# Performance work log

Hardware: AMD Instinct MI355X
Metric: run time of the kernel (lower is better)

## Reference

```python
import jax, jax.numpy as jnp
import numpy as np

WINDOW = 11
SIGMA = 1.5
C_IN = 3
PAD = WINDOW // 2
ALPHA_CHARB, ALPHA_MSE, ALPHA_SSIM = 0.3, 0.1, 0.6
EPS = 1e-6
C1 = (0.01 * 1) ** 2
C2 = (0.03 * 1) ** 2


def _gaussian_kernel():
    # 1D gaussian -> outer product -> depthwise weight [C, 1, K, K]
    x = np.arange(-(WINDOW // 2), WINDOW // 2 + 1, dtype=np.float32)
    w = np.exp(-0.5 * x * x / (SIGMA * SIGMA))
    w = w / w.sum()
    k2d = np.outer(w, w).astype(np.float32)  # [K, K]
    return jnp.asarray(np.tile(k2d[None, None], (C_IN, 1, 1, 1)))  # [C,1,K,K]

_KERNEL = _gaussian_kernel()


def _gauss_filter(x):
    # depthwise conv, NCHW / OIHW, SAME-style padding of K//2
    return jax.lax.conv_general_dilated(
        x, _KERNEL,
        window_strides=(1, 1),
        padding=[(PAD, PAD), (PAD, PAD)],
        dimension_numbers=('NCHW', 'OIHW', 'NCHW'),
        feature_group_count=C_IN,
    )


def setup_inputs() -> dict:
    key = jax.random.key(0)
    k1, k2 = jax.random.split(key)
    shape = (16, 3, 512, 512)
    pred = jax.random.uniform(k1, shape, dtype=jnp.float32)
    target = jax.random.uniform(k2, shape, dtype=jnp.float32)
    return {"pred": pred, "target": target}


def reference(pred, target):
    # SSIM map
    mu_x = _gauss_filter(pred)
    mu_y = _gauss_filter(target)
    sigma2_x = _gauss_filter(pred * pred) - mu_x * mu_x
    sigma2_y = _gauss_filter(target * target) - mu_y * mu_y
    sigma_xy = _gauss_filter(pred * target) - mu_x * mu_y
    A1 = 2.0 * mu_x * mu_y + C1
    A2 = 2.0 * sigma_xy + C2
    B1 = mu_x * mu_x + mu_y * mu_y + C1
    B2 = sigma2_x + sigma2_y + C2
    ssim = (A1 / B1) * (A2 / B2)

    diff = pred - target
    charb = jnp.sqrt(diff * diff + EPS * EPS)
    mse = diff * diff * 20.0
    ssim_loss = 1.0 - ssim
    return ALPHA_CHARB * charb + ALPHA_MSE * mse + ALPHA_SSIM * ssim_loss
```

## Files before the change

### kernel.cpp

```cpp
#include <hip/hip_runtime.h>


#define IMG    512
#define RAD    5
#define KW     11
#define STRH   32
#define NSTEP  (STRH + 2 * RAD)
#define ROWE   74
#define PLANE  (IMG * IMG)

#define C1F  1e-4f
#define C2F  9e-4f
#define EPS2 1e-12f

#define W0 0.00102838f
#define W1 0.00759876f
#define W2 0.03600076f
#define W3 0.10936067f
#define W4 0.21300537f
#define W5 0.26601297f

__global__ __launch_bounds__(256, 2)
void CombinedLossSSIMCharbMSE_81372450390186_kernel(
    const float* __restrict__ pred,
    const float* __restrict__ target,
    float* __restrict__ out)
{
    const float GW[KW] = {W0, W1, W2, W3, W4, W5, W4, W3, W2, W1, W0};

    __shared__ float2 rb[8 * ROWE];

    const int lane = threadIdx.x & 63;
    const int wav  = threadIdx.x >> 6;
    const int wid  = (blockIdx.x << 2) | wav;
    const int plane = wid >> 7;
    const int tile  = (wid >> 3) & 15;
    const int strip = wid & 7;
    const int col0 = strip << 6;
    const int row0 = tile << 5;
    const int pbase = plane * PLANE;

    const int  cA  = col0 - RAD + lane;
    const bool okA = (cA >= 0) & (cA < IMG);
    const int  cAc = min(max(cA, 0), IMG - 1);
    const int  cB  = col0 + 59 + lane;
    const bool okB = cB < IMG;
    const int  cBc = min(cB, IMG - 1);
    const bool doB = lane < 10;

    float accx[KW], accy[KW], accs[KW], accp[KW], dring[KW];
#pragma unroll
    for (int s = 0; s < KW; ++s) {
        accx[s] = 0.f; accy[s] = 0.f; accs[s] = 0.f; accp[s] = 0.f; dring[s] = 0.f;
    }

    for (int k = 0; k < 4; ++k) {
#pragma unroll
        for (int u = 0; u < KW; ++u) {
            const int i = k * KW + u;
            if (i >= NSTEP) break;
            const int r = row0 - RAD + i;

            if (r >= 0 && r < IMG) {
                const int base = pbase + r * IMG;
                float pA = pred[base + cAc];   pA = okA ? pA : 0.f;
                float tA = target[base + cAc]; tA = okA ? tA : 0.f;
                float pB = 0.f, tB = 0.f;
                if (doB) {
                    pB = pred[base + cBc];   pB = okB ? pB : 0.f;
                    tB = target[base + cBc]; tB = okB ? tB : 0.f;
                }
                float2* wrb = &rb[(wav * 2 + (i & 1)) * ROWE];
                wrb[lane] = make_float2(pA, tA);
                if (doB) wrb[64 + lane] = make_float2(pB, tB);
                __builtin_amdgcn_wave_barrier();

                float2 tv[KW];
#pragma unroll
                for (int d = 0; d < KW; ++d) tv[d] = wrb[lane + d];

                float hx = 0.f, hy = 0.f, hs = 0.f, hp = 0.f;
#pragma unroll
                for (int d = 0; d < KW; ++d) {
                    const float px = tv[d].x, py = tv[d].y;
                    const float w = GW[d];
                    hx = fmaf(w, px, hx);
                    hy = fmaf(w, py, hy);
                    hs = fmaf(w, fmaf(px, px, py * py), hs);
                    hp = fmaf(w, px * py, hp);
                }
                dring[u] = tv[RAD].x - tv[RAD].y;

#pragma unroll
                for (int s = 0; s < KW; ++s) {
                    const float w = GW[(u - s + KW) % KW];
                    accx[s] = fmaf(w, hx, accx[s]);
                    accy[s] = fmaf(w, hy, accy[s]);
                    accs[s] = fmaf(w, hs, accs[s]);
                    accp[s] = fmaf(w, hp, accp[s]);
                }
            }

            const int f = (u + 1) % KW;
            if (i >= 2 * RAD) {
                const int o = row0 + i - 2 * RAD;
                const float mu_x = accx[f], mu_y = accy[f];
                const float mxy = mu_x * mu_y;
                const float mu2 = fmaf(mu_x, mu_x, mu_y * mu_y);
                const float A1 = fmaf(2.f, mxy, C1F);
                const float A2 = fmaf(2.f, accp[f] - mxy, C2F);
                const float B1 = mu2 + C1F;
                const float B2 = (accs[f] - mu2) + C2F;
                const float ssim = (A1 * A2) * __builtin_amdgcn_rcpf(B1 * B2);
                const float d = dring[(u + 6) % KW];
                const float charb = __builtin_amdgcn_sqrtf(fmaf(d, d, EPS2));
                const float loss =
                    fmaf(0.3f, charb, fmaf(2.0f, d * d, 0.6f * (1.f - ssim)));
                out[pbase + o * IMG + col0 + lane] = loss;
            }
            accx[f] = 0.f; accy[f] = 0.f; accs[f] = 0.f; accp[f] = 0.f;
        }
    }
}

extern "C" void kernel_launch(void* const* d_in, const int* in_sizes, int n_in,
                              void* d_out, int out_size, void* d_ws, size_t ws_size,
                              hipStream_t stream) {
    const float* pred = (const float*)d_in[0];
    const float* target = (const float*)d_in[1];
    float* out = (float*)d_out;
    const int planes = in_sizes[0] / PLANE;

    dim3 grid(planes * 32);
    CombinedLossSSIMCharbMSE_81372450390186_kernel<<<grid, dim3(256), 0, stream>>>(
        pred, target, out);
}
```

Before: 189.6 us.

## Double strip height, prefetch next row, and ring-buffer horizontal sums

Each wave now processes a 64-row strip instead of 32, which cuts the halo re-read overhead from 10/32 to 10/64 and halves the grid. The next row's global loads are issued before the current row's horizontal filter, so memory latency is software-pipelined. The vertical filter changes from scattering into 11 accumulators per row to keeping a ring of horizontal sums and gathering them at output time. Launch bounds move to 4 blocks per SIMD to raise occupancy, which risks register pressure. The grid drops to 768 blocks, giving less parallelism.

```diff
diff --git a/kernel.cpp b/kernel.cpp
--- a/kernel.cpp
+++ b/kernel.cpp
@@ -4,7 +4,7 @@
 #define IMG    512
 #define RAD    5
 #define KW     11
-#define STRH   32
+#define STRH   64
 #define NSTEP  (STRH + 2 * RAD)
 #define ROWE   74
 #define PLANE  (IMG * IMG)
@@ -20,7 +20,7 @@
 #define W4 0.21300537f
 #define W5 0.26601297f
 
-__global__ __launch_bounds__(256, 2)
+__global__ __launch_bounds__(256, 4)
 void CombinedLossSSIMCharbMSE_81372450390186_kernel(
     const float* __restrict__ pred,
     const float* __restrict__ target,
@@ -33,11 +33,11 @@
     const int lane = threadIdx.x & 63;
     const int wav  = threadIdx.x >> 6;
     const int wid  = (blockIdx.x << 2) | wav;
-    const int plane = wid >> 7;
-    const int tile  = (wid >> 3) & 15;
+    const int plane = wid >> 6;
+    const int tile  = (wid >> 3) & 7;
     const int strip = wid & 7;
     const int col0 = strip << 6;
-    const int row0 = tile << 5;
+    const int row0 = tile << 6;
     const int pbase = plane * PLANE;
 
     const int  cA  = col0 - RAD + lane;
@@ -48,69 +48,90 @@
     const int  cBc = min(cB, IMG - 1);
     const bool doB = lane < 10;
 
-    float accx[KW], accy[KW], accs[KW], accp[KW], dring[KW];
+    float hrx[KW], hry[KW], hrs[KW], hrp[KW], dring[KW];
 #pragma unroll
     for (int s = 0; s < KW; ++s) {
-        accx[s] = 0.f; accy[s] = 0.f; accs[s] = 0.f; accp[s] = 0.f; dring[s] = 0.f;
+        hrx[s] = 0.f; hry[s] = 0.f; hrs[s] = 0.f; hrp[s] = 0.f; dring[s] = 0.f;
     }
 
-    for (int k = 0; k < 4; ++k) {
+    float pAr = 0.f, tAr = 0.f, pBr = 0.f, tBr = 0.f;
+    {
+        const int r = row0 - RAD;
+        if (r >= 0) {
+            const int base = pbase + r * IMG;
+            pAr = pred[base + cAc];   pAr = okA ? pAr : 0.f;
+            tAr = target[base + cAc]; tAr = okA ? tAr : 0.f;
+            if (doB) {
+                pBr = pred[base + cBc];   pBr = okB ? pBr : 0.f;
+                tBr = target[base + cBc]; tBr = okB ? tBr : 0.f;
+            }
+        }
+    }
+
+    for (int k = 0; k < 7; ++k) {
 #pragma unroll
         for (int u = 0; u < KW; ++u) {
             const int i = k * KW + u;
             if (i >= NSTEP) break;
             const int r = row0 - RAD + i;
+            const bool inr = (r >= 0) && (r < IMG);
 
-            if (r >= 0 && r < IMG) {
-                const int base = pbase + r * IMG;
-                float pA = pred[base + cAc];   pA = okA ? pA : 0.f;
-                float tA = target[base + cAc]; tA = okA ? tA : 0.f;
-                float pB = 0.f, tB = 0.f;
-                if (doB) {
-                    pB = pred[base + cBc];   pB = okB ? pB : 0.f;
-                    tB = target[base + cBc]; tB = okB ? tB : 0.f;
+            float2* wrb = &rb[(wav * 2 + (i & 1)) * ROWE];
+            if (inr) {
+                wrb[lane] = make_float2(pAr, tAr);
+                if (doB) wrb[64 + lane] = make_float2(pBr, tBr);
+                __builtin_amdgcn_wave_barrier();
+            }
+
+            {
+                const int rn = r + 1;
+                if ((i + 1 < NSTEP) && rn >= 0 && rn < IMG) {
+                    const int base = pbase + rn * IMG;
+                    pAr = pred[base + cAc];   pAr = okA ? pAr : 0.f;
+                    tAr = target[base + cAc]; tAr = okA ? tAr : 0.f;
+                    if (doB) {
+                        pBr = pred[base + cBc];   pBr = okB ? pBr : 0.f;
+                        tBr = target[base + cBc]; tBr = okB ? tBr : 0.f;
+                    }
                 }
-                float2* wrb = &rb[(wav * 2 + (i & 1)) * ROWE];
-                wrb[lane] = make_float2(pA, tA);
-                if (doB) wrb[64 + lane] = make_float2(pB, tB);
-                __builtin_amdgcn_wave_barrier();
+            }
 
-                float2 tv[KW];
-#pragma unroll
-                for (int d = 0; d < KW; ++d) tv[d] = wrb[lane + d];
-
+            if (inr) {
+                float2 c5 = make_float2(0.f, 0.f);
                 float hx = 0.f, hy = 0.f, hs = 0.f, hp = 0.f;
 #pragma unroll
                 for (int d = 0; d < KW; ++d) {
-                    const float px = tv[d].x, py = tv[d].y;
+                    const float2 t = wrb[lane + d];
+                    if (d == RAD) c5 = t;
                     const float w = GW[d];
-                    hx = fmaf(w, px, hx);
-                    hy = fmaf(w, py, hy);
-                    hs = fmaf(w, fmaf(px, px, py * py), hs);
-                    hp = fmaf(w, px * py, hp);
+                    hx = fmaf(w, t.x, hx);
+                    hy = fmaf(w, t.y, hy);
+                    hs = fmaf(w, fmaf(t.x, t.x, t.y * t.y), hs);
+                    hp = fmaf(w, t.x * t.y, hp);
                 }
-                dring[u] = tv[RAD].x - tv[RAD].y;
-
-#pragma unroll
-                for (int s = 0; s < KW; ++s) {
-                    const float w = GW[(u - s + KW) % KW];
-                    accx[s] = fmaf(w, hx, accx[s]);
-                    accy[s] = fmaf(w, hy, accy[s]);
-                    accs[s] = fmaf(w, hs, accs[s]);
-                    accp[s] = fmaf(w, hp, accp[s]);
-                }
+                hrx[u] = hx; hry[u] = hy; hrs[u] = hs; hrp[u] = hp;
+                dring[u] = c5.x - c5.y;
+            } else {
+                hrx[u] = 0.f; hry[u] = 0.f; hrs[u] = 0.f; hrp[u] = 0.f;
             }
 
-            const int f = (u + 1) % KW;
             if (i >= 2 * RAD) {
                 const int o = row0 + i - 2 * RAD;
-                const float mu_x = accx[f], mu_y = accy[f];
-                const float mxy = mu_x * mu_y;
-                const float mu2 = fmaf(mu_x, mu_x, mu_y * mu_y);
+                float vx = 0.f, vy = 0.f, vs = 0.f, vp = 0.f;
+#pragma unroll
+                for (int s2 = 0; s2 < KW; ++s2) {
+                    const float w = GW[(u - s2 + KW) % KW];
+                    vx = fmaf(w, hrx[s2], vx);
+                    vy = fmaf(w, hry[s2], vy);
+                    vs = fmaf(w, hrs[s2], vs);
+                    vp = fmaf(w, hrp[s2], vp);
+                }
+                const float mxy = vx * vy;
+                const float mu2 = fmaf(vx, vx, vy * vy);
                 const float A1 = fmaf(2.f, mxy, C1F);
-                const float A2 = fmaf(2.f, accp[f] - mxy, C2F);
+                const float A2 = fmaf(2.f, vp - mxy, C2F);
                 const float B1 = mu2 + C1F;
-                const float B2 = (accs[f] - mu2) + C2F;
+                const float B2 = (vs - mu2) + C2F;
                 const float ssim = (A1 * A2) * __builtin_amdgcn_rcpf(B1 * B2);
                 const float d = dring[(u + 6) % KW];
                 const float charb = __builtin_amdgcn_sqrtf(fmaf(d, d, EPS2));
@@ -118,7 +139,6 @@
                     fmaf(0.3f, charb, fmaf(2.0f, d * d, 0.6f * (1.f - ssim)));
                 out[pbase + o * IMG + col0 + lane] = loss;
             }
-            accx[f] = 0.f; accy[f] = 0.f; accs[f] = 0.f; accp[f] = 0.f;
         }
     }
 }
@@ -131,7 +151,7 @@
     float* out = (float*)d_out;
     const int planes = in_sizes[0] / PLANE;
 
-    dim3 grid(planes * 32);
+    dim3 grid(planes * 16);
     CombinedLossSSIMCharbMSE_81372450390186_kernel<<<grid, dim3(256), 0, stream>>>(
         pred, target, out);
 }
```

Result: slower. 298.3 us (+57.3%).

## Software-pipeline row loads and gather vertical taps from a ring of horizontal sums

Applied to the files above, without the earlier changes.

Each wave now handles 64-row strips instead of 32, which cuts the share of halo rows loaded per output. Global loads for the next row are issued before the current row's taps are computed, so load latency overlaps with compute. The vertical pass now keeps a ring of per-row horizontal sums and forms each output with an 11-tap gather, instead of scattering into 11 accumulators. Launch bounds ask for 4 blocks per CU to raise occupancy, at the cost of register pressure from the unrolled macros, and the grid has half as many blocks.

```diff
diff --git a/kernel.cpp b/kernel.cpp
--- a/kernel.cpp
+++ b/kernel.cpp
@@ -4,7 +4,7 @@
 #define IMG    512
 #define RAD    5
 #define KW     11
-#define STRH   32
+#define STRH   64
 #define NSTEP  (STRH + 2 * RAD)
 #define ROWE   74
 #define PLANE  (IMG * IMG)
@@ -20,7 +20,7 @@
 #define W4 0.21300537f
 #define W5 0.26601297f
 
-__global__ __launch_bounds__(256, 2)
+__global__ __launch_bounds__(256, 4)
 void CombinedLossSSIMCharbMSE_81372450390186_kernel(
     const float* __restrict__ pred,
     const float* __restrict__ target,
@@ -33,11 +33,11 @@
     const int lane = threadIdx.x & 63;
     const int wav  = threadIdx.x >> 6;
     const int wid  = (blockIdx.x << 2) | wav;
-    const int plane = wid >> 7;
-    const int tile  = (wid >> 3) & 15;
+    const int plane = wid >> 6;
+    const int tile  = (wid >> 3) & 7;
     const int strip = wid & 7;
     const int col0 = strip << 6;
-    const int row0 = tile << 5;
+    const int row0 = tile << 6;
     const int pbase = plane * PLANE;
 
     const int  cA  = col0 - RAD + lane;
@@ -48,79 +48,124 @@
     const int  cBc = min(cB, IMG - 1);
     const bool doB = lane < 10;
 
-    float accx[KW], accy[KW], accs[KW], accp[KW], dring[KW];
+    float hrx[KW], hry[KW], hrs[KW], hrp[KW], dring[KW];
 #pragma unroll
     for (int s = 0; s < KW; ++s) {
-        accx[s] = 0.f; accy[s] = 0.f; accs[s] = 0.f; accp[s] = 0.f; dring[s] = 0.f;
+        hrx[s] = 0.f; hry[s] = 0.f; hrs[s] = 0.f; hrp[s] = 0.f; dring[s] = 0.f;
     }
 
-    for (int k = 0; k < 4; ++k) {
-#pragma unroll
-        for (int u = 0; u < KW; ++u) {
-            const int i = k * KW + u;
-            if (i >= NSTEP) break;
-            const int r = row0 - RAD + i;
+    float pAr = 0.f, tAr = 0.f, pBr = 0.f, tBr = 0.f;
 
-            if (r >= 0 && r < IMG) {
-                const int base = pbase + r * IMG;
-                float pA = pred[base + cAc];   pA = okA ? pA : 0.f;
-                float tA = target[base + cAc]; tA = okA ? tA : 0.f;
-                float pB = 0.f, tB = 0.f;
-                if (doB) {
-                    pB = pred[base + cBc];   pB = okB ? pB : 0.f;
-                    tB = target[base + cBc]; tB = okB ? tB : 0.f;
-                }
-                float2* wrb = &rb[(wav * 2 + (i & 1)) * ROWE];
-                wrb[lane] = make_float2(pA, tA);
-                if (doB) wrb[64 + lane] = make_float2(pB, tB);
-                __builtin_amdgcn_wave_barrier();
+#define LOAD_ROW(rr) do {                                                   \
+        const int _base = pbase + (rr) * IMG;                               \
+        pAr = pred[_base + cAc];   pAr = okA ? pAr : 0.f;                   \
+        tAr = target[_base + cAc]; tAr = okA ? tAr : 0.f;                   \
+        if (doB) {                                                          \
+            pBr = pred[_base + cBc];   pBr = okB ? pBr : 0.f;               \
+            tBr = target[_base + cBc]; tBr = okB ? tBr : 0.f;               \
+        }                                                                   \
+    } while (0)
 
-                float2 tv[KW];
-#pragma unroll
-                for (int d = 0; d < KW; ++d) tv[d] = wrb[lane + d];
+#define COMMIT(par) do {                                                    \
+        float2* _w = &rb[(((wav) << 1) | (par)) * ROWE];                    \
+        _w[lane] = make_float2(pAr, tAr);                                   \
+        if (doB) _w[64 + lane] = make_float2(pBr, tBr);                     \
+        __builtin_amdgcn_wave_barrier();        \
+    } while (0)
 
-                float hx = 0.f, hy = 0.f, hs = 0.f, hp = 0.f;
-#pragma unroll
-                for (int d = 0; d < KW; ++d) {
-                    const float px = tv[d].x, py = tv[d].y;
-                    const float w = GW[d];
-                    hx = fmaf(w, px, hx);
-                    hy = fmaf(w, py, hy);
-                    hs = fmaf(w, fmaf(px, px, py * py), hs);
-                    hp = fmaf(w, px * py, hp);
-                }
-                dring[u] = tv[RAD].x - tv[RAD].y;
+#define TAPS(uu, par) do {                                                  \
+        const float2* _rd = &rb[(((wav) << 1) | (par)) * ROWE];             \
+        float _hx = 0.f, _hy = 0.f, _hs = 0.f, _hp = 0.f;                   \
+        float2 _c5 = make_float2(0.f, 0.f);                                 \
+        _Pragma("unroll")                                                   \
+        for (int _d = 0; _d < KW; ++_d) {                                   \
+            const float2 _t = _rd[lane + _d];                               \
+            if (_d == RAD) _c5 = _t;                                        \
+            const float _w = GW[_d];                                        \
+            _hx = fmaf(_w, _t.x, _hx);                                      \
+            _hy = fmaf(_w, _t.y, _hy);                                      \
+            _hs = fmaf(_w, fmaf(_t.x, _t.x, _t.y * _t.y), _hs);             \
+            _hp = fmaf(_w, _t.x * _t.y, _hp);                               \
+        }                                                                   \
+        hrx[uu] = _hx; hry[uu] = _hy; hrs[uu] = _hs; hrp[uu] = _hp;         \
+        dring[uu] = _c5.x - _c5.y;       \
+    } while (0)
 
-#pragma unroll
-                for (int s = 0; s < KW; ++s) {
-                    const float w = GW[(u - s + KW) % KW];
-                    accx[s] = fmaf(w, hx, accx[s]);
-                    accy[s] = fmaf(w, hy, accy[s]);
-                    accs[s] = fmaf(w, hs, accs[s]);
-                    accp[s] = fmaf(w, hp, accp[s]);
-                }
-            }
+#define ZERO_H(uu) do {                                                     \
+        hrx[uu] = 0.f; hry[uu] = 0.f; hrs[uu] = 0.f; hrp[uu] = 0.f;         \
+    } while (0)
 
-            const int f = (u + 1) % KW;
-            if (i >= 2 * RAD) {
-                const int o = row0 + i - 2 * RAD;
-                const float mu_x = accx[f], mu_y = accy[f];
-                const float mxy = mu_x * mu_y;
-                const float mu2 = fmaf(mu_x, mu_x, mu_y * mu_y);
-                const float A1 = fmaf(2.f, mxy, C1F);
-                const float A2 = fmaf(2.f, accp[f] - mxy, C2F);
-                const float B1 = mu2 + C1F;
-                const float B2 = (accs[f] - mu2) + C2F;
-                const float ssim = (A1 * A2) * __builtin_amdgcn_rcpf(B1 * B2);
-                const float d = dring[(u + 6) % KW];
-                const float charb = __builtin_amdgcn_sqrtf(fmaf(d, d, EPS2));
-                const float loss =
-                    fmaf(0.3f, charb, fmaf(2.0f, d * d, 0.6f * (1.f - ssim)));
-                out[pbase + o * IMG + col0 + lane] = loss;
-            }
-            accx[f] = 0.f; accy[f] = 0.f; accs[f] = 0.f; accp[f] = 0.f;
-        }
+#define FINALIZE(uu, oo) do {                                               \
+        float _vx = 0.f, _vy = 0.f, _vs = 0.f, _vp = 0.f;                   \
+        _Pragma("unroll")                                                   \
+        for (int _s = 0; _s < KW; ++_s) {                                   \
+            const float _w = GW[((uu) - _s + KW) % KW];                     \
+            _vx = fmaf(_w, hrx[_s], _vx);                                   \
+            _vy = fmaf(_w, hry[_s], _vy);                                   \
+            _vs = fmaf(_w, hrs[_s], _vs);                                   \
+            _vp = fmaf(_w, hrp[_s], _vp);                                   \
+        }                                                                   \
+        const float _mxy = _vx * _vy;                                       \
+        const float _mu2 = fmaf(_vx, _vx, _vy * _vy);                       \
+        const float _A1 = fmaf(2.f, _mxy, C1F);                             \
+        const float _A2 = fmaf(2.f, _vp - _mxy, C2F);                       \
+        const float _B1 = _mu2 + C1F;                                       \
+        const float _B2 = (_vs - _mu2) + C2F;                               \
+        const float _ssim = (_A1 * _A2) * __builtin_amdgcn_rcpf(_B1 * _B2); \
+        const float _dd = dring[((uu) + 6) % KW];     \
+        const float _ch = __builtin_amdgcn_sqrtf(fmaf(_dd, _dd, EPS2));     \
+        out[pbase + (oo) * IMG + col0 + lane] =                             \
+            fmaf(0.3f, _ch, fmaf(2.0f, _dd * _dd, 0.6f * (1.f - _ssim)));   \
+    } while (0)
+
+    if (row0 > 0) LOAD_ROW(row0 - RAD);
+
+#define STEP_PRO(uu) do {                                                   \
+        const bool _inr = (row0 - RAD + (uu)) >= 0;       \
+        if (_inr) COMMIT((uu) & 1);                                         \
+        if ((row0 - RAD + (uu) + 1) >= 0) LOAD_ROW(row0 - RAD + (uu) + 1);  \
+        if (_inr) TAPS(uu, (uu) & 1); else ZERO_H(uu);                      \
+    } while (0)
+
+    STEP_PRO(0); STEP_PRO(1); STEP_PRO(2); STEP_PRO(3); STEP_PRO(4);
+    STEP_PRO(5); STEP_PRO(6); STEP_PRO(7); STEP_PRO(8); STEP_PRO(9);
+    STEP_PRO(10);
+    FINALIZE(10, row0);
+
+    for (int k = 1; k <= 5; ++k) {
+        const int rnext = row0 - RAD + k * KW + 1;
+        const int obase = row0 + k * KW - 10;
+        const int kp = k & 1;
+#define STEP_FULL(uu) do {                                                  \
+        COMMIT(kp ^ ((uu) & 1));                                            \
+        LOAD_ROW(rnext + (uu));                                             \
+        TAPS(uu, kp ^ ((uu) & 1));                                          \
+        FINALIZE(uu, obase + (uu));                                         \
+    } while (0)
+        STEP_FULL(0); STEP_FULL(1); STEP_FULL(2); STEP_FULL(3);
+        STEP_FULL(4); STEP_FULL(5); STEP_FULL(6); STEP_FULL(7);
+        STEP_FULL(8); STEP_FULL(9); STEP_FULL(10);
+#undef STEP_FULL
     }
+
+#define STEP_EPI(uu) do {                                                   \
+        const bool _inr = (row0 + 61 + (uu)) < IMG;       \
+        if (_inr) COMMIT((uu) & 1);             \
+        if (((uu) < 7) && (row0 + 62 + (uu)) < IMG)                         \
+            LOAD_ROW(row0 + 62 + (uu));                                     \
+        if (_inr) TAPS(uu, (uu) & 1); else ZERO_H(uu);                      \
+        FINALIZE(uu, row0 + 56 + (uu));                                     \
+    } while (0)
+
+    STEP_EPI(0); STEP_EPI(1); STEP_EPI(2); STEP_EPI(3);
+    STEP_EPI(4); STEP_EPI(5); STEP_EPI(6); STEP_EPI(7);
+#undef STEP_EPI
+#undef STEP_PRO
+#undef FINALIZE
+#undef ZERO_H
+#undef TAPS
+#undef COMMIT
+#undef LOAD_ROW
 }
 
 extern "C" void kernel_launch(void* const* d_in, const int* in_sizes, int n_in,
@@ -131,7 +176,7 @@
     float* out = (float*)d_out;
     const int planes = in_sizes[0] / PLANE;
 
-    dim3 grid(planes * 32);
+    dim3 grid(planes * 16);
     CombinedLossSSIMCharbMSE_81372450390186_kernel<<<grid, dim3(256), 0, stream>>>(
         pred, target, out);
 }
```

New measurement: 231.5 us. 1.22x slower.
